# Optimization experiments

Measured on AMD Instinct MI355X. Metric: run time of the kernel, lower is better.

The kernel has to match this reference:

```python
import jax, jax.numpy as jnp
import numpy as np

N_NODES = 100000
N_EDGES = 1200000
D_IN = 64
D_OUT = 32
BN_EPS = 1e-5


def setup_inputs() -> dict:
    key = jax.random.key(0)
    ks = jax.random.split(key, 8)
    x = jax.random.normal(ks[0], (N_NODES, D_IN), dtype=jnp.float32)
    edge_index = jax.random.randint(ks[1], (2, N_EDGES), 0, N_NODES, dtype=jnp.int64)
    W1s = jax.random.normal(ks[2], (3, D_IN, D_IN), dtype=jnp.float32) * 0.05
    b1s = jax.random.normal(ks[3], (3, D_IN), dtype=jnp.float32) * 0.05
    W2s = jax.random.normal(ks[4], (3, D_IN, D_IN), dtype=jnp.float32) * 0.05
    b2s = jax.random.normal(ks[5], (3, D_IN), dtype=jnp.float32) * 0.05
    gammas = jnp.ones((3, D_IN), dtype=jnp.float32)
    betas = jnp.zeros((3, D_IN), dtype=jnp.float32)
    epss = jnp.zeros((3,), dtype=jnp.float32)  # GINConv train_eps init value 0
    lin_w = jax.random.normal(ks[6], (D_IN, D_OUT), dtype=jnp.float32) * 0.05
    lin_b = jnp.zeros((D_OUT,), dtype=jnp.float32)
    return {"x": x, "edge_index": edge_index, "W1s": W1s, "b1s": b1s,
            "W2s": W2s, "b2s": b2s, "gammas": gammas, "betas": betas,
            "epss": epss, "lin_w": lin_w, "lin_b": lin_b}


def reference(x, edge_index, W1s, b1s, W2s, b2s, gammas, betas, epss, lin_w, lin_b):
    # PyG GINConv (source_to_target): out_i = nn((1+eps)*x_i + sum_{j->i} x_j)
    src = edge_index[0]
    dst = edge_index[1]
    n = x.shape[0]
    h = x
    for i in range(3):
        agg = jax.ops.segment_sum(h[src], dst, num_segments=n)  # [N, d]
        z = (1.0 + epss[i]) * h + agg
        z = jax.nn.relu(z @ W1s[i] + b1s[i])
        z = jax.nn.relu(z @ W2s[i] + b2s[i])
        # BatchNorm1d, training mode (batch statistics, biased variance)
        mu = jnp.mean(z, axis=0)
        var = jnp.var(z, axis=0)
        z = gammas[i] * (z - mu) * jax.lax.rsqrt(var + BN_EPS) + betas[i]
        h = jax.nn.relu(z)  # F.relu after each conv
    return h @ lin_w + lin_b  # [N, D_OUT]
```

## Files before the change

kernel.cpp:

```cpp
#include <hip/hip_runtime.h>
#include <hip/hip_fp16.h>

#define NBMAX 256
#define BCAP  8192
#define CHB   3584

typedef _Float16 half8 __attribute__((ext_vector_type(8)));
typedef float f32x4 __attribute__((ext_vector_type(4)));

__device__ __forceinline__ unsigned short f2h(float f) {
    __half h = __float2half_rn(f);
    return *(unsigned short*)&h;
}

__device__ __forceinline__ int scan256(int v, int* wsum, int* woff) {
    int t = threadIdx.x, lane = t & 63, wv = t >> 6;
    int x = v;
    #pragma unroll
    for (int d = 1; d < 64; d <<= 1) {
        int y = __shfl_up(x, d, 64);
        if (lane >= d) x += y;
    }
    if (lane == 63) wsum[wv] = x;
    __syncthreads();
    if (t == 0) {
        int a = 0;
        #pragma unroll
        for (int i = 0; i < 4; ++i) { woff[i] = a; a += wsum[i]; }
    }
    __syncthreads();
    return x - v + woff[wv];
}

__global__ __launch_bounds__(256) void gin_x16init(const float* __restrict__ x,
                                                   unsigned short* __restrict__ o, int n16,
                                                   const void* __restrict__ edge,
                                                   int* __restrict__ flag,
                                                   int* __restrict__ gcount, int nb,
                                                   float* __restrict__ stats, int E) {
    if (blockIdx.x == gridDim.x - 1) {
        int t = threadIdx.x;
        for (int i = t; i < nb; i += 256) gcount[i] = 0;
        for (int i = t; i < 384; i += 256) stats[i] = 0.f;
        if (t == 0) {
            const int* p = (const int*)edge;
            int is64 = 1;
            int m = (E < 64) ? E : 64;
            for (int i = 0; i < m; ++i)
                if (p[2 * i + 1] != 0) is64 = 0;
            *flag = is64;
        }
        return;
    }
    int i = blockIdx.x * 256 + threadIdx.x;
    if (i >= n16) return;
    float4 v = ((const float4*)x)[i];
    ushort4 u;
    u.x = f2h(v.x); u.y = f2h(v.y); u.z = f2h(v.z); u.w = f2h(v.w);
    ((ushort4*)o)[i] = u;
}

__global__ __launch_bounds__(256) void gin_binscatter(const void* __restrict__ edge,
                                                      const int* __restrict__ flag,
                                                      int* __restrict__ gcount,
                                                      uint2* __restrict__ ebuf, int E, int nb) {
    __shared__ int cnt[NBMAX];
    __shared__ int dlt[NBMAX];
    __shared__ int cur[NBMAX];
    __shared__ int wsum[4], woff[4];
    __shared__ uint2 buf[CHB];
    int t = threadIdx.x;
    int beg = blockIdx.x * CHB;
    int m = E - beg; if (m > CHB) m = CHB;
    if (t < nb) cnt[t] = 0;
    __syncthreads();
    int is64 = *flag;
    for (int j = t; j < m; j += 256) {
        int e = beg + j;
        int d = is64 ? (int)((const long long*)edge)[E + e] : ((const int*)edge)[E + e];
        atomicAdd(&cnt[d >> 9], 1);
    }
    __syncthreads();
    int v = (t < nb) ? cnt[t] : 0;
    int excl = scan256(v, wsum, woff);
    if (t < nb) {
        int gb = v ? atomicAdd(&gcount[t], v) : 0;
        dlt[t] = t * BCAP + gb - excl;
        cur[t] = excl;
    }
    __syncthreads();
    for (int j = t; j < m; j += 256) {
        int e = beg + j;
        int s, d;
        if (is64) {
            s = (int)((const long long*)edge)[e];
            d = (int)((const long long*)edge)[E + e];
        } else {
            s = ((const int*)edge)[e];
            d = ((const int*)edge)[E + e];
        }
        int p = atomicAdd(&cur[d >> 9], 1);
        buf[p] = make_uint2((unsigned)s, (unsigned)d);
    }
    __syncthreads();
    for (int j = t; j < m; j += 256) {
        uint2 ed = buf[j];
        ebuf[j + dlt[(int)(ed.y >> 9)]] = ed;
    }
}

__global__ __launch_bounds__(256) void gin_build(const uint2* __restrict__ ebuf,
                                                 const int* __restrict__ gcount,
                                                 int* __restrict__ rowbeg,
                                                 int* __restrict__ rowend,
                                                 int* __restrict__ col, int n) {
    __shared__ int cnt[512];
    __shared__ int off[512];
    __shared__ int wsum[4], woff[4];
    int b = blockIdx.x, t = threadIdx.x;
    int beg = b * BCAP;
    int end = beg + gcount[b];
    cnt[t] = 0; cnt[t + 256] = 0;
    __syncthreads();
    for (int j = beg + t; j < end; j += 256)
        atomicAdd(&cnt[(int)(ebuf[j].y & 511)], 1);
    __syncthreads();
    int v0 = cnt[2 * t], v1 = cnt[2 * t + 1];
    int ep = scan256(v0 + v1, wsum, woff);
    off[2 * t] = ep;
    off[2 * t + 1] = ep + v0;
    __syncthreads();
    int node0 = b * 512 + 2 * t;
    if (node0 < n) {
        rowbeg[node0] = beg + off[2 * t];
        rowend[node0] = beg + off[2 * t] + v0;
    }
    if (node0 + 1 < n) {
        rowbeg[node0 + 1] = beg + off[2 * t + 1];
        rowend[node0 + 1] = beg + off[2 * t + 1] + v1;
    }
    __syncthreads();
    for (int j = beg + t; j < end; j += 256) {
        uint2 ed = ebuf[j];
        int p = atomicAdd(&off[(int)(ed.y & 511)], 1);
        col[beg + p] = (int)ed.x;
    }
}

template <bool APPLY>
__device__ __forceinline__ void accum8(float* acc, uint4 u,
                                       const float* sc, const float* sh) {
    float v[8];
    float2 f;
    f = __half22float2(*(const __half2*)&u.x); v[0] = f.x; v[1] = f.y;
    f = __half22float2(*(const __half2*)&u.y); v[2] = f.x; v[3] = f.y;
    f = __half22float2(*(const __half2*)&u.z); v[4] = f.x; v[5] = f.y;
    f = __half22float2(*(const __half2*)&u.w); v[6] = f.x; v[7] = f.y;
    #pragma unroll
    for (int j = 0; j < 8; ++j)
        acc[j] += APPLY ? fmaxf(fmaf(v[j], sc[j], sh[j]), 0.f) : v[j];
}

template <bool APPLY>
__device__ __forceinline__ void gather_node(const unsigned short* __restrict__ zb,
                                            int r0, int r1, int ci0,
                                            const int* __restrict__ col,
                                            float e1,
                                            const float* sc, const float* sh,
                                            _Float16* __restrict__ trow,
                                            int wid, int qn, int l16) {
    int r = l16 >> 3, c = l16 & 7;
    uint4 su = make_uint4(0, 0, 0, 0);
    if (r == 0) su = *(const uint4*)(zb + (size_t)wid * 64 + 8 * c);

    float acc[8] = {0.f, 0.f, 0.f, 0.f, 0.f, 0.f, 0.f, 0.f};
    int ci = ci0;
    for (int b2 = r0; b2 < r1; b2 += 16) {
        if (b2 > r0) {
            int ce = b2 + l16;
            ci = col[ce < r1 ? ce : r1 - 1];
        }
        uint4 u[8];
        bool p[8];
        #pragma unroll
        for (int s = 0; s < 8; ++s) {
            int j = 2 * s + r;
            p[s] = (b2 + j) < r1;
            int idx = __shfl(ci, 16 * qn + j);
            if (p[s]) u[s] = *(const uint4*)(zb + (size_t)idx * 64 + 8 * c);
        }
        #pragma unroll
        for (int s = 0; s < 8; ++s)
            if (p[s]) accum8<APPLY>(acc, u[s], sc, sh);
    }
    #pragma unroll
    for (int j = 0; j < 8; ++j)
        acc[j] += __shfl_xor(acc[j], 8);
    if (r == 0) {
        float s[8];
        float2 f;
        f = __half22float2(*(const __half2*)&su.x); s[0] = f.x; s[1] = f.y;
        f = __half22float2(*(const __half2*)&su.y); s[2] = f.x; s[3] = f.y;
        f = __half22float2(*(const __half2*)&su.z); s[4] = f.x; s[5] = f.y;
        f = __half22float2(*(const __half2*)&su.w); s[6] = f.x; s[7] = f.y;
        #pragma unroll
        for (int j = 0; j < 8; ++j) {
            float v = APPLY ? fmaxf(fmaf(s[j], sc[j], sh[j]), 0.f) : s[j];
            acc[j] = fmaf(e1, v, acc[j]);
        }
        uint4 o;
        o.x = (unsigned)f2h(acc[0]) | ((unsigned)f2h(acc[1]) << 16);
        o.y = (unsigned)f2h(acc[2]) | ((unsigned)f2h(acc[3]) << 16);
        o.z = (unsigned)f2h(acc[4]) | ((unsigned)f2h(acc[5]) << 16);
        o.w = (unsigned)f2h(acc[6]) | ((unsigned)f2h(acc[7]) << 16);
        *(uint4*)(trow + 8 * c) = o;
    }
}

template <bool APPLY>
__global__ __launch_bounds__(256, 5) void gin_fused(const unsigned short* __restrict__ zb,
                                                    const int* __restrict__ rowbeg,
                                                    const int* __restrict__ rowend,
                                                    const int* __restrict__ col,
                                                    const float* __restrict__ epss,
                                                    const float* __restrict__ gammas,
                                                    const float* __restrict__ betas,
                                                    float fN,
                                                    unsigned short* __restrict__ z16,
                                                    const float* __restrict__ W1g,
                                                    const float* __restrict__ b1g,
                                                    const float* __restrict__ W2g,
                                                    const float* __restrict__ b2g,
                                                    float* __restrict__ stats,
                                                    int layer, int n) {
    __shared__ _Float16 Wt[64 * 72];
    __shared__ _Float16 Tz[128 * 72];
    __shared__ float sS[64], sQ[64];
    __shared__ float sBN[128];
    int tid = threadIdx.x;
    int base = blockIdx.x * 128;
    const float* __restrict__ W1 = W1g + layer * 4096;
    const float* __restrict__ W2 = W2g + layer * 4096;

    for (int i = tid; i < 4096; i += 256) {
        int k = i >> 6, nn = i & 63;
        Wt[nn * 72 + k] = (_Float16)W1[i];
    }
    if (tid < 64) {
        sS[tid] = 0.f; sQ[tid] = 0.f;
        if (APPLY) {
            float mu  = stats[(layer - 1) * 128 + tid] / fN;
            float var = stats[(layer - 1) * 128 + 64 + tid] / fN - mu * mu;
            float g   = gammas[(layer - 1) * 64 + tid];
            float grs = g * rsqrtf(var + 1e-5f);
            sBN[tid]      = grs;
            sBN[64 + tid] = betas[(layer - 1) * 64 + tid] - grs * mu;
        }
    }
    __syncthreads();

    int lane = tid & 63, wv = tid >> 6;
    int qn = lane >> 4;
    int l16 = lane & 15;
    int c8 = l16 & 7;
    float e1 = 1.f + epss[layer];
    float sc[8] = {1.f, 1.f, 1.f, 1.f, 1.f, 1.f, 1.f, 1.f};
    float sh[8] = {0.f, 0.f, 0.f, 0.f, 0.f, 0.f, 0.f, 0.f};
    if (APPLY) {
        *(float4*)&sc[0] = *(const float4*)&sBN[8 * c8];
        *(float4*)&sc[4] = *(const float4*)&sBN[8 * c8 + 4];
        *(float4*)&sh[0] = *(const float4*)&sBN[64 + 8 * c8];
        *(float4*)&sh[4] = *(const float4*)&sBN[64 + 8 * c8 + 4];
    }

    int wvq = wv * 4 + qn;
    int cr0, cr1, pr0, pr1;
    {
        int w0 = base + wvq;
        cr0 = 0; cr1 = 0;
        if (w0 < n) { cr0 = rowbeg[w0]; cr1 = rowend[w0]; }
        int w1 = w0 + 16;
        pr0 = 0; pr1 = 0;
        if (w1 < n) { pr0 = rowbeg[w1]; pr1 = rowend[w1]; }
    }
    int cci = 0;
    if (cr1 > cr0) { int ce = cr0 + l16; cci = col[ce < cr1 ? ce : cr1 - 1]; }
    #pragma unroll 1
    for (int p = 0; p < 8; ++p) {
        int nci = 0;
        if (pr1 > pr0) { int ce = pr0 + l16; nci = col[ce < pr1 ? ce : pr1 - 1]; }
        int fr0 = 0, fr1 = 0;
        {
            int w2 = base + (p + 2) * 16 + wvq;
            if (p < 6 && w2 < n) { fr0 = rowbeg[w2]; fr1 = rowend[w2]; }
        }
        int widl = p * 16 + wvq;
        int wid = base + widl;
        if (wid < n) {
            gather_node<APPLY>(zb, cr0, cr1, cci, col, e1, sc, sh,
                               Tz + widl * 72, wid, qn, l16);
        } else if (l16 < 8) {
            *(uint4*)(Tz + widl * 72 + 8 * c8) = make_uint4(0u, 0u, 0u, 0u);
        }
        cr0 = pr0; cr1 = pr1; cci = nci;
        pr0 = fr0; pr1 = fr1;
    }
    __syncthreads();

    int g = qn, q = l16;
    int n0 = 32 * wv + q;
    int n1 = n0 + 16;

    half8 tb00 = *(const half8*)&Tz[n0 * 72 + 8 * g];
    half8 tb01 = *(const half8*)&Tz[n0 * 72 + 32 + 8 * g];
    half8 tb10 = *(const half8*)&Tz[n1 * 72 + 8 * g];
    half8 tb11 = *(const half8*)&Tz[n1 * 72 + 32 + 8 * g];

    f32x4 acc[2][4];
    #pragma unroll
    for (int nt = 0; nt < 2; ++nt)
        #pragma unroll
        for (int ft = 0; ft < 4; ++ft)
            acc[nt][ft] = (f32x4){0.f, 0.f, 0.f, 0.f};

    #pragma unroll
    for (int ft = 0; ft < 4; ++ft) {
        half8 a0 = *(const half8*)&Wt[(16 * ft + q) * 72 + 8 * g];
        half8 a1 = *(const half8*)&Wt[(16 * ft + q) * 72 + 32 + 8 * g];
        acc[0][ft] = __builtin_amdgcn_mfma_f32_16x16x32_f16(a0, tb00, acc[0][ft], 0, 0, 0);
        acc[0][ft] = __builtin_amdgcn_mfma_f32_16x16x32_f16(a1, tb01, acc[0][ft], 0, 0, 0);
        acc[1][ft] = __builtin_amdgcn_mfma_f32_16x16x32_f16(a0, tb10, acc[1][ft], 0, 0, 0);
        acc[1][ft] = __builtin_amdgcn_mfma_f32_16x16x32_f16(a1, tb11, acc[1][ft], 0, 0, 0);
    }

    #pragma unroll
    for (int ft = 0; ft < 4; ++ft) {
        float4 b = *(const float4*)(b1g + layer * 64 + 16 * ft + 4 * g);
        #pragma unroll
        for (int nt = 0; nt < 2; ++nt) {
            int node = nt ? n1 : n0;
            float v0 = fmaxf(acc[nt][ft][0] + b.x, 0.f);
            float v1 = fmaxf(acc[nt][ft][1] + b.y, 0.f);
            float v2 = fmaxf(acc[nt][ft][2] + b.z, 0.f);
            float v3 = fmaxf(acc[nt][ft][3] + b.w, 0.f);
            uint2 pk;
            pk.x = (unsigned)f2h(v0) | ((unsigned)f2h(v1) << 16);
            pk.y = (unsigned)f2h(v2) | ((unsigned)f2h(v3) << 16);
            *(uint2*)&Tz[node * 72 + 16 * ft + 4 * g] = pk;
        }
    }

    __syncthreads();
    for (int i = tid; i < 4096; i += 256) {
        int k = i >> 6, nn = i & 63;
        Wt[nn * 72 + k] = (_Float16)W2[i];
    }
    __syncthreads();

    half8 zb00 = *(const half8*)&Tz[n0 * 72 + 8 * g];
    half8 zb01 = *(const half8*)&Tz[n0 * 72 + 32 + 8 * g];
    half8 zb10 = *(const half8*)&Tz[n1 * 72 + 8 * g];
    half8 zb11 = *(const half8*)&Tz[n1 * 72 + 32 + 8 * g];
    #pragma unroll
    for (int nt = 0; nt < 2; ++nt)
        #pragma unroll
        for (int ft = 0; ft < 4; ++ft)
            acc[nt][ft] = (f32x4){0.f, 0.f, 0.f, 0.f};
    #pragma unroll
    for (int ft = 0; ft < 4; ++ft) {
        half8 a0 = *(const half8*)&Wt[(16 * ft + q) * 72 + 8 * g];
        half8 a1 = *(const half8*)&Wt[(16 * ft + q) * 72 + 32 + 8 * g];
        acc[0][ft] = __builtin_amdgcn_mfma_f32_16x16x32_f16(a0, zb00, acc[0][ft], 0, 0, 0);
        acc[0][ft] = __builtin_amdgcn_mfma_f32_16x16x32_f16(a1, zb01, acc[0][ft], 0, 0, 0);
        acc[1][ft] = __builtin_amdgcn_mfma_f32_16x16x32_f16(a0, zb10, acc[1][ft], 0, 0, 0);
        acc[1][ft] = __builtin_amdgcn_mfma_f32_16x16x32_f16(a1, zb11, acc[1][ft], 0, 0, 0);
    }

    #pragma unroll
    for (int ft = 0; ft < 4; ++ft) {
        float4 b = *(const float4*)(b2g + layer * 64 + 16 * ft + 4 * g);
        float s[4] = {0.f, 0.f, 0.f, 0.f};
        float sq[4] = {0.f, 0.f, 0.f, 0.f};
        #pragma unroll
        for (int nt = 0; nt < 2; ++nt) {
            int node = base + (nt ? n1 : n0);
            float v0 = fmaxf(acc[nt][ft][0] + b.x, 0.f);
            float v1 = fmaxf(acc[nt][ft][1] + b.y, 0.f);
            float v2 = fmaxf(acc[nt][ft][2] + b.z, 0.f);
            float v3 = fmaxf(acc[nt][ft][3] + b.w, 0.f);
            if (node < n) {
                s[0] += v0; sq[0] += v0 * v0;
                s[1] += v1; sq[1] += v1 * v1;
                s[2] += v2; sq[2] += v2 * v2;
                s[3] += v3; sq[3] += v3 * v3;
                uint2 pk;
                pk.x = (unsigned)f2h(v0) | ((unsigned)f2h(v1) << 16);
                pk.y = (unsigned)f2h(v2) | ((unsigned)f2h(v3) << 16);
                *(uint2*)(z16 + (size_t)node * 64 + 16 * ft + 4 * g) = pk;
            }
        }
        #pragma unroll
        for (int off = 1; off < 16; off <<= 1) {
            #pragma unroll
            for (int r2 = 0; r2 < 4; ++r2) {
                s[r2] += __shfl_xor(s[r2], off);
                sq[r2] += __shfl_xor(sq[r2], off);
            }
        }
        if (q == 0) {
            #pragma unroll
            for (int r2 = 0; r2 < 4; ++r2) {
                atomicAdd(&sS[16 * ft + 4 * g + r2], s[r2]);
                atomicAdd(&sQ[16 * ft + 4 * g + r2], sq[r2]);
            }
        }
    }
    __syncthreads();
    if (tid < 64) {
        atomicAdd(&stats[layer * 128 + tid], sS[tid]);
        atomicAdd(&stats[layer * 128 + 64 + tid], sQ[tid]);
    }
}

__global__ __launch_bounds__(256) void gin_lin(const unsigned short* __restrict__ zin,
                                               const float* __restrict__ stats,
                                               const float* __restrict__ gammas,
                                               const float* __restrict__ betas,
                                               float fN,
                                               const float* __restrict__ lw,
                                               const float* __restrict__ lb,
                                               float* __restrict__ out, int n) {
    __shared__ float Z[128 * 68];
    int tid = threadIdx.x;
    int base = blockIdx.x * 128;
    int cq = (tid & 15) * 4;
    float4 sc4, sh4;
    {
        float t0[4], t1[4];
        #pragma unroll
        for (int j = 0; j < 4; ++j) {
            int f = cq + j;
            float mu  = stats[256 + f] / fN;
            float var = stats[256 + 64 + f] / fN - mu * mu;
            float g   = gammas[128 + f];
            float grs = g * rsqrtf(var + 1e-5f);
            t0[j] = grs;
            t1[j] = betas[128 + f] - grs * mu;
        }
        sc4 = make_float4(t0[0], t0[1], t0[2], t0[3]);
        sh4 = make_float4(t1[0], t1[1], t1[2], t1[3]);
    }
    {
        const ushort4* __restrict__ src = (const ushort4*)(zin + (size_t)base * 64);
        #pragma unroll
        for (int it = 0; it < 8; ++it) {
            int idx4 = it * 256 + tid;
            int row = idx4 >> 4, c = (idx4 & 15) * 4;
            float4 v = make_float4(0.f, 0.f, 0.f, 0.f);
            if (base + row < n) {
                ushort4 u = src[idx4];
                float2 f0 = __half22float2(*(const __half2*)&u.x);
                float2 f1 = __half22float2(*(const __half2*)&u.z);
                v = make_float4(f0.x, f0.y, f1.x, f1.y);
            }
            float4 r;
            r.x = fmaxf(fmaf(v.x, sc4.x, sh4.x), 0.f);
            r.y = fmaxf(fmaf(v.y, sc4.y, sh4.y), 0.f);
            r.z = fmaxf(fmaf(v.z, sc4.z, sh4.z), 0.f);
            r.w = fmaxf(fmaf(v.w, sc4.w, sh4.w), 0.f);
            *(float4*)&Z[row * 68 + c] = r;
        }
    }
    __syncthreads();
    int tx = tid & 7, ty = tid >> 3;
    float acc[4][4];
    {
        float4 b = *(const float4*)(lb + 4 * tx);
        #pragma unroll
        for (int r = 0; r < 4; ++r) {
            acc[r][0] = b.x; acc[r][1] = b.y; acc[r][2] = b.z; acc[r][3] = b.w;
        }
    }
    #pragma unroll 4
    for (int k = 0; k < 64; ++k) {
        float4 w = *(const float4*)(lw + k * 32 + 4 * tx);
        #pragma unroll
        for (int r = 0; r < 4; ++r) {
            float a = Z[(ty + 32 * r) * 68 + k];
            acc[r][0] = fmaf(a, w.x, acc[r][0]);
            acc[r][1] = fmaf(a, w.y, acc[r][1]);
            acc[r][2] = fmaf(a, w.z, acc[r][2]);
            acc[r][3] = fmaf(a, w.w, acc[r][3]);
        }
    }
    #pragma unroll
    for (int r = 0; r < 4; ++r) {
        int row = base + ty + 32 * r;
        if (row < n) {
            float4 v;
            v.x = acc[r][0]; v.y = acc[r][1]; v.z = acc[r][2]; v.w = acc[r][3];
            *(float4*)(out + (size_t)row * 32 + 4 * tx) = v;
        }
    }
}

extern "C" void kernel_launch(void* const* d_in, const int* in_sizes, int n_in,
                              void* d_out, int out_size, void* d_ws, size_t ws_size,
                              hipStream_t stream) {
    const float* x      = (const float*)d_in[0];
    const void*  edge   = d_in[1];
    const float* W1s    = (const float*)d_in[2];
    const float* b1s    = (const float*)d_in[3];
    const float* W2s    = (const float*)d_in[4];
    const float* b2s    = (const float*)d_in[5];
    const float* gammas = (const float*)d_in[6];
    const float* betas  = (const float*)d_in[7];
    const float* epss   = (const float*)d_in[8];
    const float* lin_w  = (const float*)d_in[9];
    const float* lin_b  = (const float*)d_in[10];
    float* out = (float*)d_out;

    const int N = in_sizes[0] / 64;
    const int E = in_sizes[1] / 2;
    const int NB = (N + 511) >> 9;
    const float fN = (float)N;

    char* w = (char*)d_ws;
    auto take = [&](size_t bytes) {
        char* p = w;
        w += (bytes + 255) & ~(size_t)255;
        return p;
    };
    unsigned short* x16 = (unsigned short*)take((size_t)N * 64 * 2);
    unsigned short* hA  = (unsigned short*)take((size_t)N * 64 * 2);
    unsigned short* hB  = (unsigned short*)take((size_t)N * 64 * 2);
    uint2* ebuf    = (uint2*)take((size_t)NB * BCAP * 8);
    int*   col     = (int*)take((size_t)NB * BCAP * 4);
    int*   rowbeg  = (int*)take((size_t)N * 4);
    int*   rowend  = (int*)take((size_t)N * 4);
    int*   gcount  = (int*)take((size_t)NBMAX * 4);
    float* stats   = (float*)take(3 * 128 * 4);
    int*   flag    = (int*)take(4);

    const int n16 = N * 16;
    gin_x16init<<<(n16 + 255) / 256 + 1, 256, 0, stream>>>(x, x16, n16, edge, flag,
                                                           gcount, NB, stats, E);
    gin_binscatter<<<(E + CHB - 1) / CHB, 256, 0, stream>>>(edge, flag, gcount, ebuf, E, NB);
    gin_build<<<NB, 256, 0, stream>>>(ebuf, gcount, rowbeg, rowend, col, N);

    const int gMlp = (N + 127) / 128;
    const unsigned short* zin = x16;
    unsigned short* zout = hA;
    for (int L = 0; L < 3; ++L) {
        if (L == 0)
            gin_fused<false><<<gMlp, 256, 0, stream>>>(zin, rowbeg, rowend, col, epss,
                                                       gammas, betas, fN, zout,
                                                       W1s, b1s, W2s, b2s, stats, L, N);
        else
            gin_fused<true><<<gMlp, 256, 0, stream>>>(zin, rowbeg, rowend, col, epss,
                                                      gammas, betas, fN, zout,
                                                      W1s, b1s, W2s, b2s, stats, L, N);
        zin = zout;
        zout = (zout == hA) ? hB : hA;
    }
    gin_lin<<<gMlp, 256, 0, stream>>>(zin, stats, gammas, betas, fN, lin_w, lin_b, out, N);
}
```

Before: 318.0 us.

## Use 512-thread blocks in fused GIN layer with both weights preloaded

Doubles the block to 512 threads so each wave gathers 4 nodes instead of 8 and runs the MLP on a single 16-node tile. Both W1 and W2 are loaded into shared memory up front, which removes the mid-kernel weight reload and two block barriers. The output tile is staged in shared memory and written to global memory as coalesced 16-byte rows. The cost is more LDS per block and fewer resident blocks per CU, and the launch bounds change from (256,5) to (512,4).

```diff
diff --git a/kernel.cpp b/kernel.cpp
--- a/kernel.cpp
+++ b/kernel.cpp
@@ -218,7 +218,7 @@
 }
 
 template <bool APPLY>
-__global__ __launch_bounds__(256, 5) void gin_fused(const unsigned short* __restrict__ zb,
+__global__ __launch_bounds__(512, 4) void gin_fused(const unsigned short* __restrict__ zb,
                                                     const int* __restrict__ rowbeg,
                                                     const int* __restrict__ rowend,
                                                     const int* __restrict__ col,
@@ -233,7 +233,7 @@
                                                     const float* __restrict__ b2g,
                                                     float* __restrict__ stats,
                                                     int layer, int n) {
-    __shared__ _Float16 Wt[64 * 72];
+    __shared__ _Float16 Wt[2 * 64 * 72];
     __shared__ _Float16 Tz[128 * 72];
     __shared__ float sS[64], sQ[64];
     __shared__ float sBN[128];
@@ -242,9 +242,10 @@
     const float* __restrict__ W1 = W1g + layer * 4096;
     const float* __restrict__ W2 = W2g + layer * 4096;
 
-    for (int i = tid; i < 4096; i += 256) {
+    for (int i = tid; i < 4096; i += 512) {
         int k = i >> 6, nn = i & 63;
-        Wt[nn * 72 + k] = (_Float16)W1[i];
+        Wt[nn * 72 + k]        = (_Float16)W1[i];
+        Wt[4608 + nn * 72 + k] = (_Float16)W2[i];
     }
     if (tid < 64) {
         sS[tid] = 0.f; sQ[tid] = 0.f;
@@ -279,22 +280,22 @@
         int w0 = base + wvq;
         cr0 = 0; cr1 = 0;
         if (w0 < n) { cr0 = rowbeg[w0]; cr1 = rowend[w0]; }
-        int w1 = w0 + 16;
+        int w1 = w0 + 32;
         pr0 = 0; pr1 = 0;
         if (w1 < n) { pr0 = rowbeg[w1]; pr1 = rowend[w1]; }
     }
     int cci = 0;
     if (cr1 > cr0) { int ce = cr0 + l16; cci = col[ce < cr1 ? ce : cr1 - 1]; }
     #pragma unroll 1
-    for (int p = 0; p < 8; ++p) {
+    for (int p = 0; p < 4; ++p) {
         int nci = 0;
         if (pr1 > pr0) { int ce = pr0 + l16; nci = col[ce < pr1 ? ce : pr1 - 1]; }
         int fr0 = 0, fr1 = 0;
         {
-            int w2 = base + (p + 2) * 16 + wvq;
-            if (p < 6 && w2 < n) { fr0 = rowbeg[w2]; fr1 = rowend[w2]; }
-        }
-        int widl = p * 16 + wvq;
+            int w2 = base + (p + 2) * 32 + wvq;
+            if (p < 2 && w2 < n) { fr0 = rowbeg[w2]; fr1 = rowend[w2]; }
+        }
+        int widl = p * 32 + wvq;
         int wid = base + widl;
         if (wid < n) {
             gather_node<APPLY>(zb, cr0, cr1, cci, col, e1, sc, sh,
@@ -308,97 +309,68 @@
     __syncthreads();
 
     int g = qn, q = l16;
-    int n0 = 32 * wv + q;
-    int n1 = n0 + 16;
-
-    half8 tb00 = *(const half8*)&Tz[n0 * 72 + 8 * g];
-    half8 tb01 = *(const half8*)&Tz[n0 * 72 + 32 + 8 * g];
-    half8 tb10 = *(const half8*)&Tz[n1 * 72 + 8 * g];
-    half8 tb11 = *(const half8*)&Tz[n1 * 72 + 32 + 8 * g];
-
-    f32x4 acc[2][4];
-    #pragma unroll
-    for (int nt = 0; nt < 2; ++nt)
-        #pragma unroll
-        for (int ft = 0; ft < 4; ++ft)
-            acc[nt][ft] = (f32x4){0.f, 0.f, 0.f, 0.f};
+    int n0 = 16 * wv + q;
+
+    half8 tb0 = *(const half8*)&Tz[n0 * 72 + 8 * g];
+    half8 tb1 = *(const half8*)&Tz[n0 * 72 + 32 + 8 * g];
+
+    f32x4 acc[4];
+    #pragma unroll
+    for (int ft = 0; ft < 4; ++ft)
+        acc[ft] = (f32x4){0.f, 0.f, 0.f, 0.f};
 
     #pragma unroll
     for (int ft = 0; ft < 4; ++ft) {
         half8 a0 = *(const half8*)&Wt[(16 * ft + q) * 72 + 8 * g];
         half8 a1 = *(const half8*)&Wt[(16 * ft + q) * 72 + 32 + 8 * g];
-        acc[0][ft] = __builtin_amdgcn_mfma_f32_16x16x32_f16(a0, tb00, acc[0][ft], 0, 0, 0);
-        acc[0][ft] = __builtin_amdgcn_mfma_f32_16x16x32_f16(a1, tb01, acc[0][ft], 0, 0, 0);
-        acc[1][ft] = __builtin_amdgcn_mfma_f32_16x16x32_f16(a0, tb10, acc[1][ft], 0, 0, 0);
-        acc[1][ft] = __builtin_amdgcn_mfma_f32_16x16x32_f16(a1, tb11, acc[1][ft], 0, 0, 0);
+        acc[ft] = __builtin_amdgcn_mfma_f32_16x16x32_f16(a0, tb0, acc[ft], 0, 0, 0);
+        acc[ft] = __builtin_amdgcn_mfma_f32_16x16x32_f16(a1, tb1, acc[ft], 0, 0, 0);
     }
 
     #pragma unroll
     for (int ft = 0; ft < 4; ++ft) {
         float4 b = *(const float4*)(b1g + layer * 64 + 16 * ft + 4 * g);
-        #pragma unroll
-        for (int nt = 0; nt < 2; ++nt) {
-            int node = nt ? n1 : n0;
-            float v0 = fmaxf(acc[nt][ft][0] + b.x, 0.f);
-            float v1 = fmaxf(acc[nt][ft][1] + b.y, 0.f);
-            float v2 = fmaxf(acc[nt][ft][2] + b.z, 0.f);
-            float v3 = fmaxf(acc[nt][ft][3] + b.w, 0.f);
-            uint2 pk;
-            pk.x = (unsigned)f2h(v0) | ((unsigned)f2h(v1) << 16);
-            pk.y = (unsigned)f2h(v2) | ((unsigned)f2h(v3) << 16);
-            *(uint2*)&Tz[node * 72 + 16 * ft + 4 * g] = pk;
-        }
-    }
-
-    __syncthreads();
-    for (int i = tid; i < 4096; i += 256) {
-        int k = i >> 6, nn = i & 63;
-        Wt[nn * 72 + k] = (_Float16)W2[i];
-    }
-    __syncthreads();
-
-    half8 zb00 = *(const half8*)&Tz[n0 * 72 + 8 * g];
-    half8 zb01 = *(const half8*)&Tz[n0 * 72 + 32 + 8 * g];
-    half8 zb10 = *(const half8*)&Tz[n1 * 72 + 8 * g];
-    half8 zb11 = *(const half8*)&Tz[n1 * 72 + 32 + 8 * g];
-    #pragma unroll
-    for (int nt = 0; nt < 2; ++nt)
-        #pragma unroll
-        for (int ft = 0; ft < 4; ++ft)
-            acc[nt][ft] = (f32x4){0.f, 0.f, 0.f, 0.f};
+        float v0 = fmaxf(acc[ft][0] + b.x, 0.f);
+        float v1 = fmaxf(acc[ft][1] + b.y, 0.f);
+        float v2 = fmaxf(acc[ft][2] + b.z, 0.f);
+        float v3 = fmaxf(acc[ft][3] + b.w, 0.f);
+        uint2 pk;
+        pk.x = (unsigned)f2h(v0) | ((unsigned)f2h(v1) << 16);
+        pk.y = (unsigned)f2h(v2) | ((unsigned)f2h(v3) << 16);
+        *(uint2*)&Tz[n0 * 72 + 16 * ft + 4 * g] = pk;
+    }
+
+    half8 zb0 = *(const half8*)&Tz[n0 * 72 + 8 * g];
+    half8 zb1 = *(const half8*)&Tz[n0 * 72 + 32 + 8 * g];
+    #pragma unroll
+    for (int ft = 0; ft < 4; ++ft)
+        acc[ft] = (f32x4){0.f, 0.f, 0.f, 0.f};
     #pragma unroll
     for (int ft = 0; ft < 4; ++ft) {
-        half8 a0 = *(const half8*)&Wt[(16 * ft + q) * 72 + 8 * g];
-        half8 a1 = *(const half8*)&Wt[(16 * ft + q) * 72 + 32 + 8 * g];
-        acc[0][ft] = __builtin_amdgcn_mfma_f32_16x16x32_f16(a0, zb00, acc[0][ft], 0, 0, 0);
-        acc[0][ft] = __builtin_amdgcn_mfma_f32_16x16x32_f16(a1, zb01, acc[0][ft], 0, 0, 0);
-        acc[1][ft] = __builtin_amdgcn_mfma_f32_16x16x32_f16(a0, zb10, acc[1][ft], 0, 0, 0);
-        acc[1][ft] = __builtin_amdgcn_mfma_f32_16x16x32_f16(a1, zb11, acc[1][ft], 0, 0, 0);
-    }
-
+        half8 a0 = *(const half8*)&Wt[4608 + (16 * ft + q) * 72 + 8 * g];
+        half8 a1 = *(const half8*)&Wt[4608 + (16 * ft + q) * 72 + 32 + 8 * g];
+        acc[ft] = __builtin_amdgcn_mfma_f32_16x16x32_f16(a0, zb0, acc[ft], 0, 0, 0);
+        acc[ft] = __builtin_amdgcn_mfma_f32_16x16x32_f16(a1, zb1, acc[ft], 0, 0, 0);
+    }
+
+    int nodeg = base + n0;
     #pragma unroll
     for (int ft = 0; ft < 4; ++ft) {
         float4 b = *(const float4*)(b2g + layer * 64 + 16 * ft + 4 * g);
-        float s[4] = {0.f, 0.f, 0.f, 0.f};
-        float sq[4] = {0.f, 0.f, 0.f, 0.f};
-        #pragma unroll
-        for (int nt = 0; nt < 2; ++nt) {
-            int node = base + (nt ? n1 : n0);
-            float v0 = fmaxf(acc[nt][ft][0] + b.x, 0.f);
-            float v1 = fmaxf(acc[nt][ft][1] + b.y, 0.f);
-            float v2 = fmaxf(acc[nt][ft][2] + b.z, 0.f);
-            float v3 = fmaxf(acc[nt][ft][3] + b.w, 0.f);
-            if (node < n) {
-                s[0] += v0; sq[0] += v0 * v0;
-                s[1] += v1; sq[1] += v1 * v1;
-                s[2] += v2; sq[2] += v2 * v2;
-                s[3] += v3; sq[3] += v3 * v3;
-                uint2 pk;
-                pk.x = (unsigned)f2h(v0) | ((unsigned)f2h(v1) << 16);
-                pk.y = (unsigned)f2h(v2) | ((unsigned)f2h(v3) << 16);
-                *(uint2*)(z16 + (size_t)node * 64 + 16 * ft + 4 * g) = pk;
-            }
-        }
+        float v0 = fmaxf(acc[ft][0] + b.x, 0.f);
+        float v1 = fmaxf(acc[ft][1] + b.y, 0.f);
+        float v2 = fmaxf(acc[ft][2] + b.z, 0.f);
+        float v3 = fmaxf(acc[ft][3] + b.w, 0.f);
+        float s[4], sq[4];
+        bool ok = nodeg < n;
+        s[0] = ok ? v0 : 0.f; sq[0] = ok ? v0 * v0 : 0.f;
+        s[1] = ok ? v1 : 0.f; sq[1] = ok ? v1 * v1 : 0.f;
+        s[2] = ok ? v2 : 0.f; sq[2] = ok ? v2 * v2 : 0.f;
+        s[3] = ok ? v3 : 0.f; sq[3] = ok ? v3 * v3 : 0.f;
+        uint2 pk;
+        pk.x = (unsigned)f2h(v0) | ((unsigned)f2h(v1) << 16);
+        pk.y = (unsigned)f2h(v2) | ((unsigned)f2h(v3) << 16);
+        *(uint2*)&Tz[n0 * 72 + 16 * ft + 4 * g] = pk;
         #pragma unroll
         for (int off = 1; off < 16; off <<= 1) {
             #pragma unroll
@@ -415,6 +387,18 @@
             }
         }
     }
+
+    #pragma unroll
+    for (int t2 = 0; t2 < 2; ++t2) {
+        int u = lane + 64 * t2;
+        int rloc = 16 * wv + (u >> 3);
+        int node = base + rloc;
+        if (node < n) {
+            uint4 v = *(const uint4*)&Tz[rloc * 72 + (u & 7) * 8];
+            *(uint4*)(z16 + (size_t)node * 64 + (u & 7) * 8) = v;
+        }
+    }
+
     __syncthreads();
     if (tid < 64) {
         atomicAdd(&stats[layer * 128 + tid], sS[tid]);
@@ -553,11 +537,11 @@
     unsigned short* zout = hA;
     for (int L = 0; L < 3; ++L) {
         if (L == 0)
-            gin_fused<false><<<gMlp, 256, 0, stream>>>(zin, rowbeg, rowend, col, epss,
+            gin_fused<false><<<gMlp, 512, 0, stream>>>(zin, rowbeg, rowend, col, epss,
                                                        gammas, betas, fN, zout,
                                                        W1s, b1s, W2s, b2s, stats, L, N);
         else
-            gin_fused<true><<<gMlp, 256, 0, stream>>>(zin, rowbeg, rowend, col, epss,
+            gin_fused<true><<<gMlp, 512, 0, stream>>>(zin, rowbeg, rowend, col, epss,
                                                       gammas, betas, fN, zout,
                                                       W1s, b1s, W2s, b2s, stats, L, N);
         zin = zout;
```

Result: faster. 309.4 us (-2.7%).
